# Kernel optimization log

Measured on AMD Instinct MI355X. Metric: run time of the kernel, lower is better.

## Reference

```python
import jax, jax.numpy as jnp
import numpy as np
import math

B, N, M, D = 8, 2048, 2048, 512

def setup_inputs() -> dict:
    key = jax.random.key(0)
    ks = jax.random.split(key, 12)
    s = 1.0 / math.sqrt(D)
    return {
        "query_xyz": jax.random.normal(ks[0], (B, N, 3), jnp.float32),
        "query_feat": jax.random.normal(ks[1], (B, N, D), jnp.float32),
        "key_xyz": jax.random.normal(ks[2], (B, M, 3), jnp.float32),
        "key_feat": jax.random.normal(ks[3], (B, M, D), jnp.float32),
        "Wq": jax.random.normal(ks[4], (D, D), jnp.float32) * s,
        "bq": jnp.zeros((D,), jnp.float32),
        "Wk": jax.random.normal(ks[5], (D, D), jnp.float32) * s,
        "bk": jnp.zeros((D,), jnp.float32),
        "Wv": jax.random.normal(ks[6], (D, D), jnp.float32) * s,
        "bv": jnp.zeros((D,), jnp.float32),
        "Wo": jax.random.normal(ks[7], (D, D), jnp.float32) * s,
        "bo": jnp.zeros((D,), jnp.float32),
        "ln_g": jnp.ones((D,), jnp.float32),
        "ln_b": jnp.zeros((D,), jnp.float32),
    }

def reference(query_xyz, query_feat, key_xyz, key_feat,
              Wq, bq, Wk, bk, Wv, bv, Wo, bo, ln_g, ln_b):
    d = query_feat.shape[-1]
    # projections (torch Linear: x @ W.T + b)
    Q = jnp.einsum('bnd,ed->bne', query_feat, Wq) + bq
    K = jnp.einsum('bmd,ed->bme', key_feat, Wk) + bk
    V = jnp.einsum('bmd,ed->bme', key_feat, Wv) + bv
    scores = jnp.einsum('bnd,bmd->bnm', Q, K) / jnp.sqrt(jnp.float32(d))
    # pairwise euclidean distance via (||q||^2 + ||k||^2 - 2 q.k), avoids BxNxMx3
    qn = jnp.sum(query_xyz * query_xyz, axis=-1)  # [B,N]
    kn = jnp.sum(key_xyz * key_xyz, axis=-1)      # [B,M]
    d2 = qn[:, :, None] + kn[:, None, :] - 2.0 * jnp.einsum('bnc,bmc->bnm', query_xyz, key_xyz)
    dist = jnp.sqrt(jnp.maximum(d2, 1e-12))
    # distance bias: log(exp(-2*dist) + 1e-8)
    scores = scores + jnp.log(jnp.exp(-dist * 2.0) + 1e-8)
    attn = jax.nn.softmax(scores, axis=-1)
    # dropout is identity in eval mode
    attended = jnp.einsum('bnm,bme->bne', attn, V)
    out = jnp.einsum('bne,fe->bnf', attended, Wo) + bo
    x = query_feat + out
    # LayerNorm (eps=1e-5)
    mu = jnp.mean(x, axis=-1, keepdims=True)
    var = jnp.mean((x - mu) ** 2, axis=-1, keepdims=True)
    return (x - mu) * jax.lax.rsqrt(var + 1e-5) * ln_g + ln_b
```

## Files before the change

### kernel.cpp

```cpp
#include <hip/hip_runtime.h>

typedef __attribute__((ext_vector_type(8))) short short8;
typedef __attribute__((ext_vector_type(8))) unsigned short us8;
typedef __attribute__((ext_vector_type(4))) unsigned short us4;
typedef __attribute__((ext_vector_type(4))) float f32x4;

__device__ __forceinline__ float bf2f(unsigned short h) {
  return __uint_as_float(((unsigned int)h) << 16);
}
__device__ __forceinline__ unsigned short f2bf(float f) {
  unsigned int u = __float_as_uint(f);
  u += 0x7FFF + ((u >> 16) & 1);
  return (unsigned short)(u >> 16);
}

__device__ __forceinline__ void gload16(const void* g, void* l) {
  __builtin_amdgcn_global_load_lds(
      (const __attribute__((address_space(1))) unsigned int*)g,
      (__attribute__((address_space(3))) unsigned int*)l, 16, 0, 0);
}

#define BM 128
#define BN 128
#define BK 32

struct EpiParams {
  const float* bias;
  const float* aux0;
  const float* aux1;
  const void*  aux2;
  long  saux;
  float scale;
};

template<int EPI>
__global__ __launch_bounds__(256)
void gemm_bt(const unsigned short* __restrict__ A, const unsigned short* __restrict__ B,
             void* __restrict__ Cout, int Kd, int lda, int ldb, int ldc,
             long sA, long sB, long sC, EpiParams ep)
{
  __shared__ __attribute__((aligned(16))) char smem[16384];
  char* Al = smem;
  char* Bl = smem + 8192;

  const int t    = threadIdx.x;
  const int lane = t & 63;
  const int wid  = t >> 6;
  const int wr   = wid >> 1;
  const int wc   = wid & 1;
  const int tr   = lane & 15;
  const int tg   = lane >> 4;

  const int bz    = blockIdx.z;
  const int rbase = blockIdx.y * BM;
  const int cbase = blockIdx.x * BN;

  const unsigned short* Ab = A + (long)bz * sA;
  const unsigned short* Bb = B + (long)bz * sB;
  const char* Asrc = (const char*)(Ab + (long)rbase * lda);
  const char* Bsrc = (const char*)(Bb + (long)cbase * ldb);
  const long lda_b = (long)lda * 2;
  const long ldb_b = (long)ldb * 2;

  f32x4 acc[4][4] = {};

  for (int k0 = 0; k0 < Kd; k0 += BK) {
#pragma unroll
    for (int it = 0; it < 2; ++it) {
      const int boff = (it * 4 + wid) * 1024 + lane * 16;
      const int r  = boff >> 6;
      const int cb = boff & 63;
      gload16(Asrc + (long)r * lda_b + (k0 * 2 + cb), Al + (it * 4 + wid) * 1024);
      gload16(Bsrc + (long)r * ldb_b + (k0 * 2 + cb), Bl + (it * 4 + wid) * 1024);
    }
    __syncthreads();

    short8 af[4], bf[4];
#pragma unroll
    for (int m = 0; m < 4; ++m)
      af[m] = *(const short8*)(Al + ((wr * 64 + m * 16 + tr) * 32 + tg * 8) * 2);
#pragma unroll
    for (int n = 0; n < 4; ++n)
      bf[n] = *(const short8*)(Bl + ((wc * 64 + n * 16 + tr) * 32 + tg * 8) * 2);
#pragma unroll
    for (int m = 0; m < 4; ++m)
#pragma unroll
      for (int n = 0; n < 4; ++n)
        acc[m][n] = __builtin_amdgcn_mfma_f32_16x16x32_bf16(af[m], bf[n], acc[m][n], 0, 0, 0);
    __syncthreads();
  }

  if (EPI == 0) {
    unsigned short* C = (unsigned short*)Cout + (long)bz * sC;
#pragma unroll
    for (int n = 0; n < 4; ++n) {
      const int col = cbase + wc * 64 + n * 16 + tr;
      const float bv = ep.bias ? ep.bias[col] : 0.f;
#pragma unroll
      for (int m = 0; m < 4; ++m) {
#pragma unroll
        for (int i = 0; i < 4; ++i) {
          const int row = rbase + wr * 64 + m * 16 + tg * 4 + i;
          C[(long)row * ldc + col] = f2bf(acc[m][n][i] + bv);
        }
      }
    }
  } else {
    if (cbase < 512) {
      unsigned short* C = (unsigned short*)Cout;
#pragma unroll
      for (int n = 0; n < 4; ++n) {
        const int col = cbase + wc * 64 + n * 16 + tr;
        const float bv = ep.bias[col];
#pragma unroll
        for (int m = 0; m < 4; ++m) {
#pragma unroll
          for (int i = 0; i < 4; ++i) {
            const int row = rbase + wr * 64 + m * 16 + tg * 4 + i;
            C[(long)row * 512 + col] = f2bf(acc[m][n][i] + bv);
          }
        }
      }
    } else {
      unsigned short* C = (unsigned short*)ep.aux2;
#pragma unroll
      for (int n = 0; n < 4; ++n) {
        const int e  = cbase - 512 + wc * 64 + n * 16 + tr;
        const float bv = ep.aux1[e];
#pragma unroll
        for (int m = 0; m < 4; ++m) {
          const int row0 = rbase + wr * 64 + m * 16 + tg * 4;
          const int b  = row0 >> 11;
          const int ml = row0 & 2047;
          us4 v;
#pragma unroll
          for (int i = 0; i < 4; ++i) v[i] = f2bf(acc[m][n][i] + bv);
          *(us4*)(C + ((long)b * 512 + e) * 2048 + ml) = v;
        }
      }
    }
  }
}

template<int EPI, int NWC>
__global__ __launch_bounds__(128 * NWC, 2)
void gemm_big(const unsigned short* __restrict__ A, const unsigned short* __restrict__ B,
              void* __restrict__ Cout, int Kd, int lda, int ldb, int ldc,
              long sA, long sB, long sC, int ntn, EpiParams ep)
{
  constexpr int T  = 128 * NWC;
  constexpr int NF = 128 / (NWC * 16);
  constexpr int RA = 16384 / (T * 16);
  constexpr int RB = 8192 / (T * 16);

  __shared__ __attribute__((aligned(16))) char smem[24576];
  char* Al = smem;
  char* Bl = smem + 16384;

  const int t    = threadIdx.x;
  const int lane = t & 63;
  const int wid  = t >> 6;
  const int wr   = wid / NWC;
  const int wc   = wid % NWC;
  const int tr   = lane & 15;
  const int tg   = lane >> 4;

  const int bz    = blockIdx.x;
  const int rbase = (blockIdx.y / ntn) * 256;
  const int cbase = (blockIdx.y % ntn) * 128;

  const unsigned short* Ab = A + (long)bz * sA;
  const unsigned short* Bb = B + (long)bz * sB;
  const char* Asrc = (const char*)(Ab + (long)rbase * lda);
  const char* Bsrc = (const char*)(Bb + (long)cbase * ldb);
  const long lda_b = (long)lda * 2;
  const long ldb_b = (long)ldb * 2;

  f32x4 acc[8][NF] = {};

  for (int k0 = 0; k0 < Kd; k0 += BK) {
#pragma unroll
    for (int r = 0; r < RA; ++r) {
      const int o = (r * T + t) * 16;
      gload16(Asrc + (long)(o >> 6) * lda_b + (k0 * 2 + (o & 63)),
              Al + (r * T + wid * 64) * 16);
    }
#pragma unroll
    for (int r = 0; r < RB; ++r) {
      const int o = (r * T + t) * 16;
      gload16(Bsrc + (long)(o >> 6) * ldb_b + (k0 * 2 + (o & 63)),
              Bl + (r * T + wid * 64) * 16);
    }
    __syncthreads();

    short8 af[8], bf[NF];
#pragma unroll
    for (int m = 0; m < 8; ++m)
      af[m] = *(const short8*)(Al + ((wr * 128 + m * 16 + tr) * 32 + tg * 8) * 2);
#pragma unroll
    for (int n = 0; n < NF; ++n)
      bf[n] = *(const short8*)(Bl + ((wc * (NF * 16) + n * 16 + tr) * 32 + tg * 8) * 2);
#pragma unroll
    for (int m = 0; m < 8; ++m)
#pragma unroll
      for (int n = 0; n < NF; ++n)
        acc[m][n] = __builtin_amdgcn_mfma_f32_16x16x32_bf16(af[m], bf[n], acc[m][n], 0, 0, 0);
    __syncthreads();
  }

  if (EPI == 0) {
    float* C = (float*)Cout + (long)bz * sC;
    const float* ls = (const float*)ep.aux2 + (long)bz * 2048 + rbase;
    const float* qf = ep.aux0;
#pragma unroll
    for (int m = 0; m < 8; ++m) {
      const f32x4 lv = *(const f32x4*)(ls + wr * 128 + m * 16 + tg * 4);
      f32x4 inv;
#pragma unroll
      for (int i = 0; i < 4; ++i) inv[i] = 1.f / lv[i];
#pragma unroll
      for (int n = 0; n < NF; ++n) {
        const int col = cbase + wc * (NF * 16) + n * 16 + tr;
        const float bb = ep.bias[col];
#pragma unroll
        for (int i = 0; i < 4; ++i) {
          const int row = rbase + wr * 128 + m * 16 + tg * 4 + i;
          C[(long)row * ldc + col] =
              acc[m][n][i] * inv[i] + bb + qf[((long)bz * 2048 + row) * 512 + col];
        }
      }
    }
  } else {
    float* qs = (float*)smem;
    float* ks = (float*)smem + 768;
    {
      const float* q = ep.aux0 + (long)bz * ep.saux + (long)(rbase + t) * 3;
      qs[t * 3] = q[0]; qs[t * 3 + 1] = q[1]; qs[t * 3 + 2] = q[2];
      if (t < 128) {
        const float* k2 = ep.aux1 + (long)bz * ep.saux + (long)(cbase + t) * 3;
        ks[t * 3] = k2[0]; ks[t * 3 + 1] = k2[1]; ks[t * 3 + 2] = k2[2];
      }
    }
    __syncthreads();
    unsigned short* C = (unsigned short*)Cout + (long)bz * sC;
    float* lrow = (float*)ep.aux2 + (long)bz * 2048 + rbase;
    float ps[8][4];
#pragma unroll
    for (int m = 0; m < 8; ++m) {
#pragma unroll
      for (int i = 0; i < 4; ++i) {
        ps[m][i] = 0.f;
        const int rl = wr * 128 + m * 16 + tg * 4 + i;
        const float qx = qs[rl * 3], qy = qs[rl * 3 + 1], qz = qs[rl * 3 + 2];
#pragma unroll
        for (int n = 0; n < NF; ++n) {
          const int cl = wc * (NF * 16) + n * 16 + tr;
          const float dx = qx - ks[cl * 3];
          const float dy = qy - ks[cl * 3 + 1];
          const float dz = qz - ks[cl * 3 + 2];
          const float d2 = dx * dx + dy * dy + dz * dz;
          const float d  = sqrtf(fmaxf(d2, 1e-12f));
          const float bias = fmaxf(-2.f * d, -18.420680743952367f);
          const float p = __expf(acc[m][n][i] * ep.scale + bias - 5.f);
          ps[m][i] += p;
          C[(long)(rbase + rl) * ldc + (cbase + cl)] = f2bf(p);
        }
      }
    }
#pragma unroll
    for (int off = 1; off <= 8; off <<= 1)
#pragma unroll
      for (int m = 0; m < 8; ++m)
#pragma unroll
        for (int i = 0; i < 4; ++i)
          ps[m][i] += __shfl_xor(ps[m][i], off, 64);
    if (tr == 0) {
#pragma unroll
      for (int m = 0; m < 8; ++m)
#pragma unroll
        for (int i = 0; i < 4; ++i)
          atomicAdd(&lrow[wr * 128 + m * 16 + tg * 4 + i], ps[m][i]);
    }
  }
}

__global__ __launch_bounds__(256)
void ln_rows(const float* __restrict__ X, const float* __restrict__ g,
             const float* __restrict__ b, float* __restrict__ O)
{
  const int row  = blockIdx.x * 4 + (threadIdx.x >> 6);
  const int lane = threadIdx.x & 63;
  const float* xp = X + (long)row * 512;

  f32x4 v0 = *(const f32x4*)(xp + lane * 4);
  f32x4 v1 = *(const f32x4*)(xp + 256 + lane * 4);

  float s = 0.f;
#pragma unroll
  for (int j = 0; j < 4; ++j) s += v0[j] + v1[j];
#pragma unroll
  for (int off = 32; off; off >>= 1) s += __shfl_xor(s, off, 64);
  const float mu = s * (1.f / 512.f);

  float vs = 0.f;
#pragma unroll
  for (int j = 0; j < 4; ++j) {
    float d0 = v0[j] - mu, d1 = v1[j] - mu;
    vs += d0 * d0 + d1 * d1;
  }
#pragma unroll
  for (int off = 32; off; off >>= 1) vs += __shfl_xor(vs, off, 64);
  const float r = rsqrtf(vs * (1.f / 512.f) + 1e-5f);

  f32x4 g0 = *(const f32x4*)(g + lane * 4);
  f32x4 g1 = *(const f32x4*)(g + 256 + lane * 4);
  f32x4 b0 = *(const f32x4*)(b + lane * 4);
  f32x4 b1 = *(const f32x4*)(b + 256 + lane * 4);

  f32x4 o0, o1;
#pragma unroll
  for (int j = 0; j < 4; ++j) {
    o0[j] = (v0[j] - mu) * r * g0[j] + b0[j];
    o1[j] = (v1[j] - mu) * r * g1[j] + b1[j];
  }
  float* op = O + (long)row * 512;
  *(f32x4*)(op + lane * 4) = o0;
  *(f32x4*)(op + 256 + lane * 4) = o1;
}

__global__ __launch_bounds__(256)
void cvt_feat(const float* __restrict__ a, const float* __restrict__ b,
              unsigned short* __restrict__ oa, unsigned short* __restrict__ ob)
{
  const float* src = blockIdx.y ? b : a;
  unsigned short* dst = blockIdx.y ? ob : oa;
  const long i = blockIdx.x * 256 + threadIdx.x;
  const f32x4* s = (const f32x4*)src;
  f32x4 x = s[i * 2];
  f32x4 y = s[i * 2 + 1];
  us8 o;
#pragma unroll
  for (int j = 0; j < 4; ++j) { o[j] = f2bf(x[j]); o[4 + j] = f2bf(y[j]); }
  *(us8*)(dst + i * 8) = o;
}

__global__ __launch_bounds__(256)
void cvt_w(const float* __restrict__ w0, const float* __restrict__ w1,
           const float* __restrict__ w2, const float* __restrict__ w3,
           unsigned short* __restrict__ dst)
{
  const float* src = blockIdx.y == 0 ? w0 : blockIdx.y == 1 ? w1 : blockIdx.y == 2 ? w2 : w3;
  unsigned short* d = dst + (long)blockIdx.y * 262144;
  const long i = blockIdx.x * 256 + threadIdx.x;
  const f32x4* s = (const f32x4*)src;
  f32x4 x = s[i * 2];
  f32x4 y = s[i * 2 + 1];
  us8 o;
#pragma unroll
  for (int j = 0; j < 4; ++j) { o[j] = f2bf(x[j]); o[4 + j] = f2bf(y[j]); }
  *(us8*)(d + i * 8) = o;
}

__global__ __launch_bounds__(256)
void cvt_wT(const float* __restrict__ Wv, unsigned short* __restrict__ WvT)
{
  __shared__ float tile[64 * 68];
  const int t = threadIdx.x;
  const int e0 = blockIdx.y * 64, d0 = blockIdx.x * 64;
#pragma unroll
  for (int c = 0; c < 4; ++c) {
    const int L = c * 256 + t;
    const int r = L >> 4, g = L & 15;
    const f32x4 v = *(const f32x4*)(Wv + (long)(e0 + r) * 512 + d0 + g * 4);
    *(f32x4*)(tile + r * 68 + g * 4) = v;
  }
  __syncthreads();
#pragma unroll
  for (int c = 0; c < 2; ++c) {
    const int L = c * 256 + t;
    const int d = L >> 3, ge = L & 7;
    us8 o;
#pragma unroll
    for (int j = 0; j < 8; ++j) o[j] = f2bf(tile[(ge * 8 + j) * 68 + d]);
    *(us8*)(WvT + (long)(d0 + d) * 512 + e0 + ge * 8) = o;
  }
}

__global__ __launch_bounds__(256)
void bvo_k(const float* __restrict__ Wo, const float* __restrict__ bv,
           float* __restrict__ out)
{
  const int f = blockIdx.x * 256 + threadIdx.x;
  float s = 0.f;
  for (int e = 0; e < 512; e += 4) {
    const f32x4 w = *(const f32x4*)(Wo + (long)f * 512 + e);
    const f32x4 b = *(const f32x4*)(bv + e);
    s += w[0] * b[0] + w[1] * b[1] + w[2] * b[2] + w[3] * b[3];
  }
  out[f] = s;
}

extern "C" void kernel_launch(void* const* d_in, const int* in_sizes, int n_in,
                              void* d_out, int out_size, void* d_ws, size_t ws_size,
                              hipStream_t stream)
{
  const float* qxyz  = (const float*)d_in[0];
  const float* qfeat = (const float*)d_in[1];
  const float* kxyz  = (const float*)d_in[2];
  const float* kfeat = (const float*)d_in[3];
  const float* Wq = (const float*)d_in[4];
  const float* bq = (const float*)d_in[5];
  const float* Wk = (const float*)d_in[6];
  const float* bk = (const float*)d_in[7];
  const float* Wv = (const float*)d_in[8];
  const float* bv = (const float*)d_in[9];
  const float* Wo = (const float*)d_in[10];
  const float* bo = (const float*)d_in[11];
  const float* lng = (const float*)d_in[12];
  const float* lnb = (const float*)d_in[13];

  const long SZ_FEAT = 16777216;
  char* ws = (char*)d_ws;
  if (ws_size < (size_t)153092096) return;

  unsigned short* XQ  = (unsigned short*)(ws);
  unsigned short* XK  = (unsigned short*)(ws + SZ_FEAT);
  unsigned short* QB  = (unsigned short*)(ws + 2 * SZ_FEAT);
  unsigned short* KB  = (unsigned short*)(ws + 3 * SZ_FEAT);
  unsigned short* VT  = (unsigned short*)(ws + 4 * SZ_FEAT);
  unsigned short* WQB = (unsigned short*)(ws + 5 * SZ_FEAT);
  unsigned short* WKB = WQB + 262144;
  unsigned short* WVO = WQB + 524288;
  unsigned short* WOB = WQB + 786432;
  unsigned short* SB  = (unsigned short*)(ws + 5 * SZ_FEAT + 2097152);
  unsigned short* WVT = SB;
  float* BVO  = (float*)((char*)SB + 524288);
  float* XRES = (float*)ws;
  float* LSUM = (float*)(WOB);

  cvt_feat<<<dim3(4096, 2), 256, 0, stream>>>(qfeat, kfeat, XQ, XK);
  cvt_w<<<dim3(128, 4), 256, 0, stream>>>(Wq, Wk, Wv, Wo, WQB);
  cvt_wT<<<dim3(8, 8), 256, 0, stream>>>(Wv, WVT);
  bvo_k<<<dim3(2), 256, 0, stream>>>(Wo, bv, BVO);

  EpiParams ew{};
  gemm_bt<0><<<dim3(4, 4, 1), 256, 0, stream>>>(WOB, WVT, WVO, 512, 512, 512, 512, 0, 0, 0, ew);

  EpiParams e0{}; e0.bias = bq;
  gemm_bt<0><<<dim3(4, 128, 1), 256, 0, stream>>>(XQ, WQB, QB, 512, 512, 512, 512, 0, 0, 0, e0);
  EpiParams e1{}; e1.bias = bk; e1.aux1 = BVO; e1.aux2 = VT;
  gemm_bt<4><<<dim3(8, 128, 1), 256, 0, stream>>>(XK, WKB, KB, 512, 512, 512, 512, 0, 0, 0, e1);

  hipMemsetAsync(LSUM, 0, 8 * 2048 * sizeof(float), stream);

  EpiParams es{}; es.aux0 = qxyz; es.aux1 = kxyz; es.aux2 = LSUM; es.saux = 2048 * 3;
  es.scale = 0.044194173824159216f;
  gemm_big<2, 2><<<dim3(8, 128), 256, 0, stream>>>(QB, KB, SB, 512, 512, 512, 2048,
                                                   (long)2048 * 512, (long)2048 * 512,
                                                   (long)2048 * 2048, 16, es);

  EpiParams ep{}; ep.aux2 = LSUM; ep.bias = bo; ep.aux0 = qfeat;
  gemm_big<0, 4><<<dim3(8, 32), 512, 0, stream>>>(SB, VT, XRES, 2048, 2048, 2048, 512,
                                                  (long)2048 * 2048, (long)512 * 2048,
                                                  (long)2048 * 512, 4, ep);

  ln_rows<<<4096, 256, 0, stream>>>(XRES, lng, lnb, (float*)d_out);
}
```

Baseline: 287.6 us.

## Replace big GEMMs with 256x256 double-buffered, swizzled 8-wave pipelined kernel

Replaces the two large attention GEMMs (QK^T scores and PV) with a new kernel that uses 256x256 tiles, 8 waves, BK=64 and two LDS buffers of 64KB. Global-to-LDS loads for the next k-tile are issued in quarters between MFMA phases, and the LDS layout is XOR-swizzled to avoid bank conflicts. s_setprio is raised around the MFMA bursts. The goal is to hide memory latency and raise data reuse per block. In exchange it uses about 134KB of LDS, which allows one block per CU, launches fewer blocks, and relies on hand-placed waitcnt and barriers being correct.

```diff
diff --git a/kernel.cpp b/kernel.cpp
--- a/kernel.cpp
+++ b/kernel.cpp
@@ -142,85 +142,143 @@
   }
 }
 
-template<int EPI, int NWC>
-__global__ __launch_bounds__(128 * NWC, 2)
-void gemm_big(const unsigned short* __restrict__ A, const unsigned short* __restrict__ B,
-              void* __restrict__ Cout, int Kd, int lda, int ldb, int ldc,
-              long sA, long sB, long sC, int ntn, EpiParams ep)
-{
-  constexpr int T  = 128 * NWC;
-  constexpr int NF = 128 / (NWC * 16);
-  constexpr int RA = 16384 / (T * 16);
-  constexpr int RB = 8192 / (T * 16);
-
-  __shared__ __attribute__((aligned(16))) char smem[24576];
-  char* Al = smem;
-  char* Bl = smem + 16384;
+template<int EPI>
+__global__ __launch_bounds__(512, 1)
+void gemm8p(const unsigned short* __restrict__ A, const unsigned short* __restrict__ B,
+            void* __restrict__ Cout, int Kd, int lda, int ldb, int ldc,
+            long sA, long sB, long sC, int ntn, EpiParams ep)
+{
+  __shared__ __attribute__((aligned(16))) char smem[137216];
 
   const int t    = threadIdx.x;
   const int lane = t & 63;
   const int wid  = t >> 6;
-  const int wr   = wid / NWC;
-  const int wc   = wid % NWC;
+  const int wr   = wid >> 2;
+  const int wc   = wid & 3;
   const int tr   = lane & 15;
   const int tg   = lane >> 4;
 
   const int bz    = blockIdx.x;
   const int rbase = (blockIdx.y / ntn) * 256;
-  const int cbase = (blockIdx.y % ntn) * 128;
-
-  const unsigned short* Ab = A + (long)bz * sA;
-  const unsigned short* Bb = B + (long)bz * sB;
-  const char* Asrc = (const char*)(Ab + (long)rbase * lda);
-  const char* Bsrc = (const char*)(Bb + (long)cbase * ldb);
+  const int cbase = (blockIdx.y % ntn) * 256;
+
   const long lda_b = (long)lda * 2;
   const long ldb_b = (long)ldb * 2;
-
-  f32x4 acc[8][NF] = {};
-
-  for (int k0 = 0; k0 < Kd; k0 += BK) {
-#pragma unroll
-    for (int r = 0; r < RA; ++r) {
-      const int o = (r * T + t) * 16;
-      gload16(Asrc + (long)(o >> 6) * lda_b + (k0 * 2 + (o & 63)),
-              Al + (r * T + wid * 64) * 16);
-    }
-#pragma unroll
-    for (int r = 0; r < RB; ++r) {
-      const int o = (r * T + t) * 16;
-      gload16(Bsrc + (long)(o >> 6) * ldb_b + (k0 * 2 + (o & 63)),
-              Bl + (r * T + wid * 64) * 16);
-    }
-    __syncthreads();
-
-    short8 af[8], bf[NF];
-#pragma unroll
-    for (int m = 0; m < 8; ++m)
-      af[m] = *(const short8*)(Al + ((wr * 128 + m * 16 + tr) * 32 + tg * 8) * 2);
-#pragma unroll
-    for (int n = 0; n < NF; ++n)
-      bf[n] = *(const short8*)(Bl + ((wc * (NF * 16) + n * 16 + tr) * 32 + tg * 8) * 2);
-#pragma unroll
-    for (int m = 0; m < 8; ++m)
-#pragma unroll
-      for (int n = 0; n < NF; ++n)
-        acc[m][n] = __builtin_amdgcn_mfma_f32_16x16x32_bf16(af[m], bf[n], acc[m][n], 0, 0, 0);
-    __syncthreads();
-  }
+  const char* Asrc = (const char*)(A + (long)bz * sA + (long)rbase * lda);
+  const char* Bsrc = (const char*)(B + (long)bz * sB + (long)cbase * ldb);
+
+  const int srow = t >> 3;
+  const int sg   = (t & 7) ^ ((t >> 3) & 7);
+
+  if (EPI == 2) {
+    float* qs  = (float*)(smem + 131072);
+    float* ks2 = (float*)(smem + 131072 + 3072);
+    if (t < 256) {
+      const float* q = ep.aux0 + (long)bz * ep.saux + (long)(rbase + t) * 3;
+      qs[t * 3] = q[0]; qs[t * 3 + 1] = q[1]; qs[t * 3 + 2] = q[2];
+    } else {
+      const int tt = t - 256;
+      const float* k2 = ep.aux1 + (long)bz * ep.saux + (long)(cbase + tt) * 3;
+      ks2[tt * 3] = k2[0]; ks2[tt * 3 + 1] = k2[1]; ks2[tt * 3 + 2] = k2[2];
+    }
+  }
+
+#define STAGEH(mat, h, tk, sb) {                                              \
+    char* _d = smem + (sb) + (mat) * 32768 + (h) * 16384 + wid * 1024;        \
+    const long _ldx = (mat) ? ldb_b : lda_b;                                  \
+    const char* _s = ((mat) ? Bsrc : Asrc) + (long)((h) * 128 + srow) * _ldx  \
+                     + (long)(tk) * 128 + sg * 16;                            \
+    gload16(_s, _d);                                                          \
+    gload16(_s + 64 * _ldx, _d + 8192); }
+
+#define RDA(sb, mh)                                                           \
+    _Pragma("unroll") for (int mm = 0; mm < 4; ++mm) {                        \
+      const int lr = (mh) * 64 + mm * 16 + tr;                                \
+      _Pragma("unroll") for (int ks = 0; ks < 2; ++ks)                        \
+        af[mm][ks] = *(const short8*)(smem + (sb) + Ab0 + lr * 128 +          \
+                       (((ks * 4 + tg) ^ (lr & 7)) << 4)); }
+
+#define RDB(sb, nh)                                                           \
+    _Pragma("unroll") for (int nn = 0; nn < 2; ++nn) {                        \
+      const int lbr = lbr0 + ((nh) * 2 + nn) * 16 + tr;                       \
+      _Pragma("unroll") for (int ks = 0; ks < 2; ++ks)                        \
+        bf[(nh) * 2 + nn][ks] = *(const short8*)(smem + (sb) + 32768 + Bh0 +  \
+                       lbr * 128 + (((ks * 4 + tg) ^ (lbr & 7)) << 4)); }
+
+#define MFQ(mh, nh)                                                           \
+    __builtin_amdgcn_s_setprio(1);                                            \
+    _Pragma("unroll") for (int mm = 0; mm < 4; ++mm)                          \
+    _Pragma("unroll") for (int nn = 0; nn < 2; ++nn)                          \
+    _Pragma("unroll") for (int ks = 0; ks < 2; ++ks)                          \
+      acc[(mh) * 4 + mm][(nh) * 2 + nn] = __builtin_amdgcn_mfma_f32_16x16x32_bf16( \
+          af[mm][ks], bf[(nh) * 2 + nn][ks], acc[(mh) * 4 + mm][(nh) * 2 + nn], 0, 0, 0); \
+    __builtin_amdgcn_s_setprio(0);
+
+#define BAR   __builtin_amdgcn_s_barrier()
+#define LGKM0 asm volatile("s_waitcnt lgkmcnt(0)" ::: "memory")
+
+  const int Ab0  = wr * 16384;
+  const int Bh0  = (wc >> 1) * 16384;
+  const int lbr0 = (wc & 1) * 64;
+
+  f32x4 acc[8][4] = {};
+  short8 af[4][2], bf[4][2];
+  const int NT = Kd >> 6;
+
+  STAGEH(1, 0, 0, 0) STAGEH(0, 0, 0, 0) STAGEH(0, 1, 0, 0) STAGEH(1, 1, 0, 0)
+  STAGEH(1, 0, 1, 65536) STAGEH(0, 0, 1, 65536)
+  asm volatile("s_waitcnt vmcnt(4)" ::: "memory");
+  BAR;
+
+#pragma unroll 1
+  for (int i2 = 0; i2 < NT; i2 += 2) {
+    const bool more = (i2 + 2 < NT);
+    RDA(0, 0) RDB(0, 0)
+    STAGEH(0, 1, i2 + 1, 65536)
+    BAR; LGKM0; MFQ(0, 0) BAR;
+    RDB(0, 1)
+    STAGEH(1, 1, i2 + 1, 65536)
+    BAR; LGKM0; MFQ(0, 1) BAR;
+    RDA(0, 1)
+    if (more) STAGEH(1, 0, i2 + 2, 0)
+    BAR; LGKM0; MFQ(1, 1) BAR;
+    if (more) STAGEH(0, 0, i2 + 2, 0)
+    BAR; LGKM0; MFQ(1, 0)
+    if (more) { asm volatile("s_waitcnt vmcnt(4)" ::: "memory"); }
+    else      { asm volatile("s_waitcnt vmcnt(0)" ::: "memory"); }
+    BAR;
+    RDA(65536, 0) RDB(65536, 0)
+    if (more) STAGEH(0, 1, i2 + 2, 0)
+    BAR; LGKM0; MFQ(0, 0) BAR;
+    RDB(65536, 1)
+    if (more) STAGEH(1, 1, i2 + 2, 0)
+    BAR; LGKM0; MFQ(0, 1) BAR;
+    RDA(65536, 1)
+    if (more) STAGEH(1, 0, i2 + 3, 65536)
+    BAR; LGKM0; MFQ(1, 1) BAR;
+    if (more) STAGEH(0, 0, i2 + 3, 65536)
+    BAR; LGKM0; MFQ(1, 0)
+    if (more) { asm volatile("s_waitcnt vmcnt(4)" ::: "memory"); }
+    BAR;
+  }
+#undef STAGEH
+#undef RDA
+#undef RDB
+#undef MFQ
 
   if (EPI == 0) {
     float* C = (float*)Cout + (long)bz * sC;
-    const float* ls = (const float*)ep.aux2 + (long)bz * 2048 + rbase;
+    const float* ls = (const float*)ep.aux2 + (long)bz * 2048 + rbase + wr * 128;
     const float* qf = ep.aux0;
 #pragma unroll
     for (int m = 0; m < 8; ++m) {
-      const f32x4 lv = *(const f32x4*)(ls + wr * 128 + m * 16 + tg * 4);
+      const f32x4 lv = *(const f32x4*)(ls + m * 16 + tg * 4);
       f32x4 inv;
 #pragma unroll
       for (int i = 0; i < 4; ++i) inv[i] = 1.f / lv[i];
 #pragma unroll
-      for (int n = 0; n < NF; ++n) {
-        const int col = cbase + wc * (NF * 16) + n * 16 + tr;
+      for (int n = 0; n < 4; ++n) {
+        const int col = cbase + wc * 64 + n * 16 + tr;
         const float bb = ep.bias[col];
 #pragma unroll
         for (int i = 0; i < 4; ++i) {
@@ -231,17 +289,8 @@
       }
     }
   } else {
-    float* qs = (float*)smem;
-    float* ks = (float*)smem + 768;
-    {
-      const float* q = ep.aux0 + (long)bz * ep.saux + (long)(rbase + t) * 3;
-      qs[t * 3] = q[0]; qs[t * 3 + 1] = q[1]; qs[t * 3 + 2] = q[2];
-      if (t < 128) {
-        const float* k2 = ep.aux1 + (long)bz * ep.saux + (long)(cbase + t) * 3;
-        ks[t * 3] = k2[0]; ks[t * 3 + 1] = k2[1]; ks[t * 3 + 2] = k2[2];
-      }
-    }
-    __syncthreads();
+    const float* qs  = (const float*)(smem + 131072);
+    const float* ks2 = (const float*)(smem + 131072 + 3072);
     unsigned short* C = (unsigned short*)Cout + (long)bz * sC;
     float* lrow = (float*)ep.aux2 + (long)bz * 2048 + rbase;
     float ps[8][4];
@@ -253,11 +302,11 @@
         const int rl = wr * 128 + m * 16 + tg * 4 + i;
         const float qx = qs[rl * 3], qy = qs[rl * 3 + 1], qz = qs[rl * 3 + 2];
 #pragma unroll
-        for (int n = 0; n < NF; ++n) {
-          const int cl = wc * (NF * 16) + n * 16 + tr;
-          const float dx = qx - ks[cl * 3];
-          const float dy = qy - ks[cl * 3 + 1];
-          const float dz = qz - ks[cl * 3 + 2];
+        for (int n = 0; n < 4; ++n) {
+          const int cl = wc * 64 + n * 16 + tr;
+          const float dx = qx - ks2[cl * 3];
+          const float dy = qy - ks2[cl * 3 + 1];
+          const float dz = qz - ks2[cl * 3 + 2];
           const float d2 = dx * dx + dy * dy + dz * dz;
           const float d  = sqrtf(fmaxf(d2, 1e-12f));
           const float bias = fmaxf(-2.f * d, -18.420680743952367f);
@@ -455,14 +504,14 @@
 
   EpiParams es{}; es.aux0 = qxyz; es.aux1 = kxyz; es.aux2 = LSUM; es.saux = 2048 * 3;
   es.scale = 0.044194173824159216f;
-  gemm_big<2, 2><<<dim3(8, 128), 256, 0, stream>>>(QB, KB, SB, 512, 512, 512, 2048,
-                                                   (long)2048 * 512, (long)2048 * 512,
-                                                   (long)2048 * 2048, 16, es);
+  gemm8p<2><<<dim3(8, 64), 512, 0, stream>>>(QB, KB, SB, 512, 512, 512, 2048,
+                                             (long)2048 * 512, (long)2048 * 512,
+                                             (long)2048 * 2048, 8, es);
 
   EpiParams ep{}; ep.aux2 = LSUM; ep.bias = bo; ep.aux0 = qfeat;
-  gemm_big<0, 4><<<dim3(8, 32), 512, 0, stream>>>(SB, VT, XRES, 2048, 2048, 2048, 512,
-                                                  (long)2048 * 2048, (long)512 * 2048,
-                                                  (long)2048 * 512, 4, ep);
+  gemm8p<0><<<dim3(8, 16), 512, 0, stream>>>(SB, VT, XRES, 2048, 2048, 2048, 512,
+                                             (long)2048 * 2048, (long)512 * 2048,
+                                             (long)2048 * 512, 2, ep);
 
   ln_rows<<<4096, 256, 0, stream>>>(XRES, lng, lnb, (float*)d_out);
 }
```

New measurement: 293.0 us. No clear change (+1.9%).

## Replace atomic row-sum with partial buffers; move Q/K projections to larger-tile GEMM

Applied to the files above, without the earlier changes.

Softmax denominators are no longer accumulated with global atomics into a memset-zeroed buffer. Each score block now writes per-column-tile partial sums, and the LayerNorm kernel reduces them, then applies the 1/sum scale, output bias and residual. The Q and K/V projections switch from the 128x128 gemm_bt to the 256-row gemm_big tiles, with the batch folded into the z/stride logic. This removes the memset and atomic contention and lightens the PV GEMM epilogue, at the cost of an extra residual read inside the LN kernel.

```diff
diff --git a/kernel.cpp b/kernel.cpp
--- a/kernel.cpp
+++ b/kernel.cpp
@@ -33,11 +33,9 @@
   float scale;
 };
 
-template<int EPI>
 __global__ __launch_bounds__(256)
 void gemm_bt(const unsigned short* __restrict__ A, const unsigned short* __restrict__ B,
-             void* __restrict__ Cout, int Kd, int lda, int ldb, int ldc,
-             long sA, long sB, long sC, EpiParams ep)
+             unsigned short* __restrict__ C, int Kd, int lda, int ldb, int ldc)
 {
   __shared__ __attribute__((aligned(16))) char smem[16384];
   char* Al = smem;
@@ -51,14 +49,11 @@
   const int tr   = lane & 15;
   const int tg   = lane >> 4;
 
-  const int bz    = blockIdx.z;
   const int rbase = blockIdx.y * BM;
   const int cbase = blockIdx.x * BN;
 
-  const unsigned short* Ab = A + (long)bz * sA;
-  const unsigned short* Bb = B + (long)bz * sB;
-  const char* Asrc = (const char*)(Ab + (long)rbase * lda);
-  const char* Bsrc = (const char*)(Bb + (long)cbase * ldb);
+  const char* Asrc = (const char*)(A + (long)rbase * lda);
+  const char* Bsrc = (const char*)(B + (long)cbase * ldb);
   const long lda_b = (long)lda * 2;
   const long ldb_b = (long)ldb * 2;
 
@@ -90,53 +85,15 @@
     __syncthreads();
   }
 
-  if (EPI == 0) {
-    unsigned short* C = (unsigned short*)Cout + (long)bz * sC;
-#pragma unroll
-    for (int n = 0; n < 4; ++n) {
-      const int col = cbase + wc * 64 + n * 16 + tr;
-      const float bv = ep.bias ? ep.bias[col] : 0.f;
-#pragma unroll
-      for (int m = 0; m < 4; ++m) {
-#pragma unroll
-        for (int i = 0; i < 4; ++i) {
-          const int row = rbase + wr * 64 + m * 16 + tg * 4 + i;
-          C[(long)row * ldc + col] = f2bf(acc[m][n][i] + bv);
-        }
-      }
-    }
-  } else {
-    if (cbase < 512) {
-      unsigned short* C = (unsigned short*)Cout;
-#pragma unroll
-      for (int n = 0; n < 4; ++n) {
-        const int col = cbase + wc * 64 + n * 16 + tr;
-        const float bv = ep.bias[col];
-#pragma unroll
-        for (int m = 0; m < 4; ++m) {
-#pragma unroll
-          for (int i = 0; i < 4; ++i) {
-            const int row = rbase + wr * 64 + m * 16 + tg * 4 + i;
-            C[(long)row * 512 + col] = f2bf(acc[m][n][i] + bv);
-          }
-        }
-      }
-    } else {
-      unsigned short* C = (unsigned short*)ep.aux2;
-#pragma unroll
-      for (int n = 0; n < 4; ++n) {
-        const int e  = cbase - 512 + wc * 64 + n * 16 + tr;
-        const float bv = ep.aux1[e];
-#pragma unroll
-        for (int m = 0; m < 4; ++m) {
-          const int row0 = rbase + wr * 64 + m * 16 + tg * 4;
-          const int b  = row0 >> 11;
-          const int ml = row0 & 2047;
-          us4 v;
-#pragma unroll
-          for (int i = 0; i < 4; ++i) v[i] = f2bf(acc[m][n][i] + bv);
-          *(us4*)(C + ((long)b * 512 + e) * 2048 + ml) = v;
-        }
+#pragma unroll
+  for (int n = 0; n < 4; ++n) {
+    const int col = cbase + wc * 64 + n * 16 + tr;
+#pragma unroll
+    for (int m = 0; m < 4; ++m) {
+#pragma unroll
+      for (int i = 0; i < 4; ++i) {
+        const int row = rbase + wr * 64 + m * 16 + tg * 4 + i;
+        C[(long)row * ldc + col] = f2bf(acc[m][n][i]);
       }
     }
   }
@@ -208,25 +165,64 @@
     __syncthreads();
   }
 
-  if (EPI == 0) {
+  if (EPI == 1) {
     float* C = (float*)Cout + (long)bz * sC;
-    const float* ls = (const float*)ep.aux2 + (long)bz * 2048 + rbase;
-    const float* qf = ep.aux0;
 #pragma unroll
     for (int m = 0; m < 8; ++m) {
-      const f32x4 lv = *(const f32x4*)(ls + wr * 128 + m * 16 + tg * 4);
-      f32x4 inv;
-#pragma unroll
-      for (int i = 0; i < 4; ++i) inv[i] = 1.f / lv[i];
+#pragma unroll
+      for (int n = 0; n < NF; ++n) {
+        const int col = cbase + wc * (NF * 16) + n * 16 + tr;
+#pragma unroll
+        for (int i = 0; i < 4; ++i) {
+          const int row = rbase + wr * 128 + m * 16 + tg * 4 + i;
+          C[(long)row * ldc + col] = acc[m][n][i];
+        }
+      }
+    }
+  } else if (EPI == 5) {
+    unsigned short* C = (unsigned short*)Cout + (long)bz * sC;
+#pragma unroll
+    for (int n = 0; n < NF; ++n) {
+      const int col = cbase + wc * (NF * 16) + n * 16 + tr;
+      const float bb = ep.bias[col];
+#pragma unroll
+      for (int m = 0; m < 8; ++m) {
+#pragma unroll
+        for (int i = 0; i < 4; ++i) {
+          const int row = rbase + wr * 128 + m * 16 + tg * 4 + i;
+          C[(long)row * ldc + col] = f2bf(acc[m][n][i] + bb);
+        }
+      }
+    }
+  } else if (EPI == 6) {
+    if (cbase < 512) {
+      unsigned short* C = (unsigned short*)Cout + (long)bz * sC;
 #pragma unroll
       for (int n = 0; n < NF; ++n) {
         const int col = cbase + wc * (NF * 16) + n * 16 + tr;
         const float bb = ep.bias[col];
 #pragma unroll
-        for (int i = 0; i < 4; ++i) {
-          const int row = rbase + wr * 128 + m * 16 + tg * 4 + i;
-          C[(long)row * ldc + col] =
-              acc[m][n][i] * inv[i] + bb + qf[((long)bz * 2048 + row) * 512 + col];
+        for (int m = 0; m < 8; ++m) {
+#pragma unroll
+          for (int i = 0; i < 4; ++i) {
+            const int row = rbase + wr * 128 + m * 16 + tg * 4 + i;
+            C[(long)row * 512 + col] = f2bf(acc[m][n][i] + bb);
+          }
+        }
+      }
+    } else {
+      unsigned short* C = (unsigned short*)ep.aux2;
+#pragma unroll
+      for (int n = 0; n < NF; ++n) {
+        const int e  = cbase - 512 + wc * (NF * 16) + n * 16 + tr;
+        const float bb = ep.aux1[e];
+#pragma unroll
+        for (int m = 0; m < 8; ++m) {
+          const int row0 = rbase + wr * 128 + m * 16 + tg * 4;
+          us4 v;
+#pragma unroll
+          for (int i = 0; i < 4; ++i) v[i] = f2bf(acc[m][n][i] + bb);
+          *(us4*)(C + ((long)bz * 512 + e) * 2048 + row0) = v;
         }
       }
     }
@@ -243,7 +239,6 @@
     }
     __syncthreads();
     unsigned short* C = (unsigned short*)Cout + (long)bz * sC;
-    float* lrow = (float*)ep.aux2 + (long)bz * 2048 + rbase;
     float ps[8][4];
 #pragma unroll
     for (int m = 0; m < 8; ++m) {
@@ -274,30 +269,58 @@
 #pragma unroll
         for (int i = 0; i < 4; ++i)
           ps[m][i] += __shfl_xor(ps[m][i], off, 64);
+    float* sPart = (float*)(smem + 8192);
     if (tr == 0) {
 #pragma unroll
       for (int m = 0; m < 8; ++m)
 #pragma unroll
         for (int i = 0; i < 4; ++i)
-          atomicAdd(&lrow[wr * 128 + m * 16 + tg * 4 + i], ps[m][i]);
-    }
-  }
-}
-
-__global__ __launch_bounds__(256)
-void ln_rows(const float* __restrict__ X, const float* __restrict__ g,
-             const float* __restrict__ b, float* __restrict__ O)
+          sPart[wc * 256 + wr * 128 + m * 16 + tg * 4 + i] = ps[m][i];
+    }
+    __syncthreads();
+    if (t < 256) {
+      float* lp = (float*)ep.aux2 +
+                  (long)bz * 32768 + (long)(blockIdx.y % ntn) * 2048 + rbase + t;
+      *lp = sPart[t] + sPart[256 + t];
+    }
+  }
+}
+
+__global__ __launch_bounds__(256)
+void ln_rows(const float* __restrict__ X, const float* __restrict__ LPART,
+             const float* __restrict__ qf, const float* __restrict__ bo,
+             const float* __restrict__ g, const float* __restrict__ b,
+             float* __restrict__ O)
 {
   const int row  = blockIdx.x * 4 + (threadIdx.x >> 6);
   const int lane = threadIdx.x & 63;
+  const int bz   = row >> 11;
+  const int rl   = row & 2047;
+
+  float p = LPART[(long)bz * 32768 + (long)(lane & 15) * 2048 + rl];
+#pragma unroll
+  for (int off = 1; off <= 8; off <<= 1) p += __shfl_xor(p, off, 64);
+  const float inv = 1.f / p;
+
   const float* xp = X + (long)row * 512;
-
-  f32x4 v0 = *(const f32x4*)(xp + lane * 4);
-  f32x4 v1 = *(const f32x4*)(xp + 256 + lane * 4);
+  const float* qp = qf + (long)row * 512;
+
+  f32x4 x0 = *(const f32x4*)(xp + lane * 4);
+  f32x4 x1 = *(const f32x4*)(xp + 256 + lane * 4);
+  const f32x4 q0 = *(const f32x4*)(qp + lane * 4);
+  const f32x4 q1 = *(const f32x4*)(qp + 256 + lane * 4);
+  const f32x4 o0b = *(const f32x4*)(bo + lane * 4);
+  const f32x4 o1b = *(const f32x4*)(bo + 256 + lane * 4);
+
+#pragma unroll
+  for (int j = 0; j < 4; ++j) {
+    x0[j] = x0[j] * inv + o0b[j] + q0[j];
+    x1[j] = x1[j] * inv + o1b[j] + q1[j];
+  }
 
   float s = 0.f;
 #pragma unroll
-  for (int j = 0; j < 4; ++j) s += v0[j] + v1[j];
+  for (int j = 0; j < 4; ++j) s += x0[j] + x1[j];
 #pragma unroll
   for (int off = 32; off; off >>= 1) s += __shfl_xor(s, off, 64);
   const float mu = s * (1.f / 512.f);
@@ -305,23 +328,23 @@
   float vs = 0.f;
 #pragma unroll
   for (int j = 0; j < 4; ++j) {
-    float d0 = v0[j] - mu, d1 = v1[j] - mu;
+    float d0 = x0[j] - mu, d1 = x1[j] - mu;
     vs += d0 * d0 + d1 * d1;
   }
 #pragma unroll
   for (int off = 32; off; off >>= 1) vs += __shfl_xor(vs, off, 64);
   const float r = rsqrtf(vs * (1.f / 512.f) + 1e-5f);
 
-  f32x4 g0 = *(const f32x4*)(g + lane * 4);
-  f32x4 g1 = *(const f32x4*)(g + 256 + lane * 4);
-  f32x4 b0 = *(const f32x4*)(b + lane * 4);
-  f32x4 b1 = *(const f32x4*)(b + 256 + lane * 4);
+  const f32x4 g0 = *(const f32x4*)(g + lane * 4);
+  const f32x4 g1 = *(const f32x4*)(g + 256 + lane * 4);
+  const f32x4 b0 = *(const f32x4*)(b + lane * 4);
+  const f32x4 b1 = *(const f32x4*)(b + 256 + lane * 4);
 
   f32x4 o0, o1;
 #pragma unroll
   for (int j = 0; j < 4; ++j) {
-    o0[j] = (v0[j] - mu) * r * g0[j] + b0[j];
-    o1[j] = (v1[j] - mu) * r * g1[j] + b1[j];
+    o0[j] = (x0[j] - mu) * r * g0[j] + b0[j];
+    o1[j] = (x1[j] - mu) * r * g1[j] + b1[j];
   }
   float* op = O + (long)row * 512;
   *(f32x4*)(op + lane * 4) = o0;
@@ -436,33 +459,32 @@
   unsigned short* WVT = SB;
   float* BVO  = (float*)((char*)SB + 524288);
   float* XRES = (float*)ws;
-  float* LSUM = (float*)(WOB);
+  float* LPART = (float*)WQB;
 
   cvt_feat<<<dim3(4096, 2), 256, 0, stream>>>(qfeat, kfeat, XQ, XK);
   cvt_w<<<dim3(128, 4), 256, 0, stream>>>(Wq, Wk, Wv, Wo, WQB);
   cvt_wT<<<dim3(8, 8), 256, 0, stream>>>(Wv, WVT);
   bvo_k<<<dim3(2), 256, 0, stream>>>(Wo, bv, BVO);
 
-  EpiParams ew{};
-  gemm_bt<0><<<dim3(4, 4, 1), 256, 0, stream>>>(WOB, WVT, WVO, 512, 512, 512, 512, 0, 0, 0, ew);
+  gemm_bt<<<dim3(4, 4), 256, 0, stream>>>(WOB, WVT, WVO, 512, 512, 512, 512);
 
   EpiParams e0{}; e0.bias = bq;
-  gemm_bt<0><<<dim3(4, 128, 1), 256, 0, stream>>>(XQ, WQB, QB, 512, 512, 512, 512, 0, 0, 0, e0);
+  gemm_big<5, 2><<<dim3(8, 32), 256, 0, stream>>>(XQ, WQB, QB, 512, 512, 512, 512,
+                                                  (long)2048 * 512, 0, (long)2048 * 512, 4, e0);
   EpiParams e1{}; e1.bias = bk; e1.aux1 = BVO; e1.aux2 = VT;
-  gemm_bt<4><<<dim3(8, 128, 1), 256, 0, stream>>>(XK, WKB, KB, 512, 512, 512, 512, 0, 0, 0, e1);
-
-  hipMemsetAsync(LSUM, 0, 8 * 2048 * sizeof(float), stream);
-
-  EpiParams es{}; es.aux0 = qxyz; es.aux1 = kxyz; es.aux2 = LSUM; es.saux = 2048 * 3;
+  gemm_big<6, 2><<<dim3(8, 64), 256, 0, stream>>>(XK, WKB, KB, 512, 512, 512, 512,
+                                                  (long)2048 * 512, 0, (long)2048 * 512, 8, e1);
+
+  EpiParams es{}; es.aux0 = qxyz; es.aux1 = kxyz; es.aux2 = LPART; es.saux = 2048 * 3;
   es.scale = 0.044194173824159216f;
   gemm_big<2, 2><<<dim3(8, 128), 256, 0, stream>>>(QB, KB, SB, 512, 512, 512, 2048,
                                                    (long)2048 * 512, (long)2048 * 512,
                                                    (long)2048 * 2048, 16, es);
 
-  EpiParams ep{}; ep.aux2 = LSUM; ep.bias = bo; ep.aux0 = qfeat;
-  gemm_big<0, 4><<<dim3(8, 32), 512, 0, stream>>>(SB, VT, XRES, 2048, 2048, 2048, 512,
+  EpiParams ep{};
+  gemm_big<1, 4><<<dim3(8, 32), 512, 0, stream>>>(SB, VT, XRES, 2048, 2048, 2048, 512,
                                                   (long)2048 * 2048, (long)512 * 2048,
                                                   (long)2048 * 512, 4, ep);
 
-  ln_rows<<<4096, 256, 0, stream>>>(XRES, lng, lnb, (float*)d_out);
-}
+  ln_rows<<<4096, 256, 0, stream>>>(XRES, LPART, qfeat, bo, lng, lnb, (float*)d_out);
+}
```

Measured after the change: 267.9 us. -6.8%, faster.
